# Optimization experiments

Measured on AMD Instinct MI355X. Metric: run time of the kernel, lower is better.

Reference implementation:

```python
import jax, jax.numpy as jnp
import numpy as np

OUT = 128
TYPES = [("author", 100000, 128), ("paper", 250000, 256), ("venue", 25000, 64),
         ("institution", 50000, 128), ("field", 75000, 64), ("term", 150000, 128)]


def setup_inputs() -> dict:
    key = jax.random.key(0)
    inp = {}
    for i, (name, n, f_in) in enumerate(TYPES):
        kx, kw, kb = jax.random.split(jax.random.fold_in(key, i), 3)
        inp[f"x_{name}"] = jax.random.normal(kx, (n, f_in), dtype=jnp.float32)
        # kaiming_uniform default init of torch Linear: bound = 1/sqrt(fan_in)
        bound = 1.0 / np.sqrt(f_in)
        inp[f"W_{name}"] = jax.random.uniform(kw, (OUT, f_in), dtype=jnp.float32, minval=-bound, maxval=bound)
        inp[f"b_{name}"] = jax.random.uniform(kb, (OUT,), dtype=jnp.float32, minval=-bound, maxval=bound)
    return inp


def reference(x_author, x_paper, x_venue, x_institution, x_field, x_term,
              W_author, b_author, W_paper, b_paper, W_venue, b_venue,
              W_institution, b_institution, W_field, b_field, W_term, b_term):
    # Per-type independent Linear: y_k = x_k @ W_k^T + b_k (grouped GEMM)
    def lin(x, W, b):
        return jnp.einsum('nf,of->no', x, W) + b
    return (lin(x_author, W_author, b_author),
            lin(x_paper, W_paper, b_paper),
            lin(x_venue, W_venue, b_venue),
            lin(x_institution, W_institution, b_institution),
            lin(x_field, W_field, b_field),
            lin(x_term, W_term, b_term))
```

## Files before the change

### kernel.cpp

```cpp
#include <hip/hip_runtime.h>

typedef __bf16 bf16x8 __attribute__((ext_vector_type(8)));
typedef float  f32x4  __attribute__((ext_vector_type(4)));

struct KArgs {
    const float* x[6];
    const float* W[6];
    const float* b[6];
    float*       out[6];
    int nrows[6];
    int blk0[7];
};

template<int N> __device__ __forceinline__ void wait_bar() {
    asm volatile("s_waitcnt vmcnt(%0)\n\ts_barrier" :: "n"(N) : "memory");
}
__device__ __forceinline__ void order_fence() { asm volatile("" ::: "memory"); }

__device__ __forceinline__ void gload_lds16(const float* g, void* l) {
    __builtin_amdgcn_global_load_lds(
        (const __attribute__((address_space(1))) void*)g,
        (__attribute__((address_space(3))) void*)l, 16, 0, 0);
}

template<int FIN, bool GUARD>
__device__ __forceinline__ void compute_chunk(
    const char* __restrict__ base, const bf16x8 (&Wf)[FIN/32][2],
    const f32x4 (&bv)[2], float* __restrict__ out, int nrows, int chunk,
    int l15, int lq, int colbase)
{
    constexpr int ROWS = 4096 / FIN;
    constexpr int NC   = FIN / 32;
    constexpr int MT   = ROWS / 16;
    constexpr int R    = FIN / 4;
    #pragma unroll
    for (int mt = 0; mt < MT; ++mt) {
        const int row = mt * 16 + l15;
        const int swz = row & 7;
        f32x4 acc0 = {0.f, 0.f, 0.f, 0.f};
        f32x4 acc1 = {0.f, 0.f, 0.f, 0.f};
        #pragma unroll
        for (int c = 0; c < NC; ++c) {
            const int g0 = row * R + c * 8 + lq * 2;
            const f32x4 lo = *(const f32x4*)(base + (size_t)((g0 ^ swz) << 4));
            const f32x4 hi = *(const f32x4*)(base + (size_t)(((g0 + 1) ^ swz) << 4));
            bf16x8 xf;
            xf[0]=(__bf16)lo[0]; xf[1]=(__bf16)lo[1]; xf[2]=(__bf16)lo[2]; xf[3]=(__bf16)lo[3];
            xf[4]=(__bf16)hi[0]; xf[5]=(__bf16)hi[1]; xf[6]=(__bf16)hi[2]; xf[7]=(__bf16)hi[3];
            acc0 = __builtin_amdgcn_mfma_f32_16x16x32_bf16(Wf[c][0], xf, acc0, 0, 0, 0);
            acc1 = __builtin_amdgcn_mfma_f32_16x16x32_bf16(Wf[c][1], xf, acc1, 0, 0, 0);
        }
        const int xrow = chunk * ROWS + mt * 16 + l15;
        if (!GUARD || xrow < nrows) {
            float* op = out + (size_t)xrow * 128 + colbase;
            *(f32x4*)(op + lq * 4)      = acc0 + bv[0];
            *(f32x4*)(op + 16 + lq * 4) = acc1 + bv[1];
        }
    }
}

template<int FIN>
__device__ __forceinline__ void run_type(
    const float* __restrict__ x, const float* __restrict__ W,
    const float* __restrict__ bias, float* __restrict__ out,
    int nrows, int c0, int c1, bool tail, float* __restrict__ lds)
{
    constexpr int ROWS = 4096 / FIN;
    constexpr int NC   = FIN / 32;
    constexpr int MT   = ROWS / 16;
    constexpr int R    = FIN / 4;
    constexpr int S    = 2 * MT;
    constexpr int LOGR = (FIN == 256) ? 6 : ((FIN == 128) ? 5 : 4);

    const int tid     = threadIdx.x;
    const int lane    = tid & 63;
    const int wave    = tid >> 6;
    const int l15     = lane & 15;
    const int lq      = lane >> 4;
    const int colbase = wave * 32;

    bf16x8 Wf[NC][2];
    f32x4  bv[2];
    #pragma unroll
    for (int t = 0; t < 2; ++t) {
        const int o = colbase + t * 16 + l15;
        #pragma unroll
        for (int c = 0; c < NC; ++c) {
            const f32x4 w0 = *(const f32x4*)(W + (size_t)o * FIN + c * 32 + lq * 8);
            const f32x4 w1 = *(const f32x4*)(W + (size_t)o * FIN + c * 32 + lq * 8 + 4);
            bf16x8 fr;
            fr[0]=(__bf16)w0[0]; fr[1]=(__bf16)w0[1]; fr[2]=(__bf16)w0[2]; fr[3]=(__bf16)w0[3];
            fr[4]=(__bf16)w1[0]; fr[5]=(__bf16)w1[1]; fr[6]=(__bf16)w1[2]; fr[7]=(__bf16)w1[3];
            Wf[c][t] = fr;
        }
        bv[t] = *(const f32x4*)(bias + colbase + t * 16 + lq * 4);
    }

    auto issue = [&](int chunk, int b) {
        const float* src = x + (size_t)chunk * ROWS * FIN;
        #pragma unroll
        for (int i = 0; i < 4; ++i) {
            const int G   = wave * 256 + i * 64 + lane;
            const int row = G >> LOGR;
            const int kq  = (G & (R - 1)) ^ (row & 7);
            gload_lds16(src + (size_t)row * FIN + kq * 4,
                        (char*)lds + (size_t)b * 16384 + wave * 4096 + i * 1024);
        }
    };

    const int L = c1 - c0;
    if (L > 0) {
        const int last = c1 - 1;
        order_fence();
        issue(c0, 0);
        int ch1 = c0 + 1; if (ch1 > last) ch1 = last;
        issue(ch1, 1);
        wait_bar<4>();
        int ch2 = c0 + 2; if (ch2 > last) ch2 = last;
        issue(ch2, 2);
        order_fence();
        compute_chunk<FIN, false>((const char*)lds, Wf, bv, out, nrows, c0,
                                  l15, lq, colbase);
        if (L > 1) {
            wait_bar<4 + S>();
            for (int k = 1; k < L; ++k) {
                int ch = c0 + k + 2; if (ch > last) ch = last;
                issue(ch, (k + 2) % 3);
                order_fence();
                compute_chunk<FIN, false>((const char*)lds + (size_t)(k % 3) * 16384,
                                          Wf, bv, out, nrows, c0 + k,
                                          l15, lq, colbase);
                if (k + 1 < L) wait_bar<4 + 2 * S>();
            }
        }
    }

    if (tail) {
        __syncthreads();
        const int pc = c1;
        #pragma unroll
        for (int i = 0; i < 4; ++i) {
            const int G   = wave * 256 + i * 64 + lane;
            const int row = G >> LOGR;
            const int kq  = (G & (R - 1)) ^ (row & 7);
            const int grow = pc * ROWS + row;
            if (grow < nrows) {
                const f32x4 v = *(const f32x4*)(x + (size_t)grow * FIN + kq * 4);
                *(f32x4*)((char*)lds + (size_t)G * 16) = v;
            }
        }
        __syncthreads();
        compute_chunk<FIN, true>((const char*)lds, Wf, bv, out, nrows, pc,
                                 l15, lq, colbase);
    }
}

__global__ __launch_bounds__(256, 3) void hetero_fused_kern(KArgs A)
{
    __shared__ float lds[3 * 4096];

    int ty = 0;
    const int bid = blockIdx.x;
    while (ty < 5 && bid >= A.blk0[ty + 1]) ++ty;
    const int lb = bid - A.blk0[ty];
    const int nb = A.blk0[ty + 1] - A.blk0[ty];

    const int nrows = A.nrows[ty];
    const int ROWS  = (ty == 1) ? 16 : ((ty == 2 || ty == 4) ? 64 : 32);
    const int F     = nrows / ROWS;
    const bool part = (nrows % ROWS) != 0;
    const int c0 = (int)(((long)F * lb) / nb);
    const int c1 = (int)(((long)F * (lb + 1)) / nb);
    const bool tail = part && (lb == nb - 1);

    switch (ty) {
        case 0: run_type<128>(A.x[0], A.W[0], A.b[0], A.out[0], nrows, c0, c1, tail, lds); break;
        case 1: run_type<256>(A.x[1], A.W[1], A.b[1], A.out[1], nrows, c0, c1, tail, lds); break;
        case 2: run_type< 64>(A.x[2], A.W[2], A.b[2], A.out[2], nrows, c0, c1, tail, lds); break;
        case 3: run_type<128>(A.x[3], A.W[3], A.b[3], A.out[3], nrows, c0, c1, tail, lds); break;
        case 4: run_type< 64>(A.x[4], A.W[4], A.b[4], A.out[4], nrows, c0, c1, tail, lds); break;
        case 5: run_type<128>(A.x[5], A.W[5], A.b[5], A.out[5], nrows, c0, c1, tail, lds); break;
    }
}

extern "C" void kernel_launch(void* const* d_in, const int* in_sizes, int n_in,
                              void* d_out, int out_size, void* d_ws, size_t ws_size,
                              hipStream_t stream)
{
    float* out = (float*)d_out;
    KArgs A;
    const int  nrows[6] = {100000, 250000, 25000, 50000, 75000, 150000};
    const long ooff[6]  = {0L, 12800000L, 44800000L, 48000000L, 54400000L, 64000000L};
    const int  blk0[7]  = {0, 273, 1297, 1348, 1485, 1639, 2048};
    for (int t = 0; t < 6; ++t) {
        A.x[t]     = (const float*)d_in[3 * t + 0];
        A.W[t]     = (const float*)d_in[3 * t + 1];
        A.b[t]     = (const float*)d_in[3 * t + 2];
        A.out[t]   = out + ooff[t];
        A.nrows[t] = nrows[t];
    }
    for (int i = 0; i < 7; ++i) A.blk0[i] = blk0[i];

    hetero_fused_kern<<<2048, 256, 0, stream>>>(A);
}
```

Measured before the change: 165.3 us.

## Split each block into producer and consumer waves for warp-specialised pipelining

Blocks grow to 512 threads. Four producer waves only stream x chunks into the triple-buffered LDS ring with global_load_lds, and four consumer waves hold the bf16 weight fragments and run the MFMA compute and stores. The aim is to stop each wave alternating between issuing loads and computing, so loads and math overlap more cleanly. The grid is halved to 1024 blocks and the per-type block offsets are rescaled to match. The cost is more LDS barriers per chunk, fewer compute waves per CU, and register or LDS limits that may hold occupancy below the launch-bounds target.

```diff
diff --git a/kernel.cpp b/kernel.cpp
--- a/kernel.cpp
+++ b/kernel.cpp
@@ -12,10 +12,12 @@
     int blk0[7];
 };
 
-template<int N> __device__ __forceinline__ void wait_bar() {
-    asm volatile("s_waitcnt vmcnt(%0)\n\ts_barrier" :: "n"(N) : "memory");
-}
-__device__ __forceinline__ void order_fence() { asm volatile("" ::: "memory"); }
+__device__ __forceinline__ void prod_wait_bar() {
+    asm volatile("s_waitcnt vmcnt(4)\n\ts_barrier" ::: "memory");
+}
+__device__ __forceinline__ void cons_bar() {
+    asm volatile("s_waitcnt lgkmcnt(0)\n\ts_barrier" ::: "memory");
+}
 
 __device__ __forceinline__ void gload_lds16(const float* g, void* l) {
     __builtin_amdgcn_global_load_lds(
@@ -67,71 +69,71 @@
 {
     constexpr int ROWS = 4096 / FIN;
     constexpr int NC   = FIN / 32;
-    constexpr int MT   = ROWS / 16;
     constexpr int R    = FIN / 4;
-    constexpr int S    = 2 * MT;
     constexpr int LOGR = (FIN == 256) ? 6 : ((FIN == 128) ? 5 : 4);
 
-    const int tid     = threadIdx.x;
-    const int lane    = tid & 63;
-    const int wave    = tid >> 6;
-    const int l15     = lane & 15;
-    const int lq      = lane >> 4;
-    const int colbase = wave * 32;
-
-    bf16x8 Wf[NC][2];
-    f32x4  bv[2];
-    #pragma unroll
-    for (int t = 0; t < 2; ++t) {
-        const int o = colbase + t * 16 + l15;
+    const int tid  = threadIdx.x;
+    const int lane = tid & 63;
+    const int wave = tid >> 6;
+    const int l15  = lane & 15;
+    const int lq   = lane >> 4;
+    const bool is_prod = (wave < 4);
+
+    const int L    = c1 - c0;
+    const int last = c1 - 1;
+
+    if (is_prod) {
+        const int pw = wave;
+        auto issue = [&](int chunk, int slot) {
+            const float* src = x + (size_t)chunk * ROWS * FIN;
+            #pragma unroll
+            for (int i = 0; i < 4; ++i) {
+                const int G   = pw * 256 + i * 64 + lane;
+                const int row = G >> LOGR;
+                const int kq  = (G & (R - 1)) ^ (row & 7);
+                gload_lds16(src + (size_t)row * FIN + kq * 4,
+                            (char*)lds + (size_t)slot * 16384 + pw * 4096 + i * 1024);
+            }
+        };
+        if (L > 0) {
+            issue(c0, c0 % 3);
+            int ch1 = c0 + 1; if (ch1 > last) ch1 = last;
+            issue(ch1, (c0 + 1) % 3);
+            prod_wait_bar();
+            for (int k = c0; k < c1; ++k) {
+                int ch = k + 2; if (ch > last) ch = last;
+                issue(ch, (k + 2) % 3);
+                prod_wait_bar();
+            }
+        }
+    } else {
+        const int colbase = (wave - 4) * 32;
+        bf16x8 Wf[NC][2];
+        f32x4  bv[2];
         #pragma unroll
-        for (int c = 0; c < NC; ++c) {
-            const f32x4 w0 = *(const f32x4*)(W + (size_t)o * FIN + c * 32 + lq * 8);
-            const f32x4 w1 = *(const f32x4*)(W + (size_t)o * FIN + c * 32 + lq * 8 + 4);
-            bf16x8 fr;
-            fr[0]=(__bf16)w0[0]; fr[1]=(__bf16)w0[1]; fr[2]=(__bf16)w0[2]; fr[3]=(__bf16)w0[3];
-            fr[4]=(__bf16)w1[0]; fr[5]=(__bf16)w1[1]; fr[6]=(__bf16)w1[2]; fr[7]=(__bf16)w1[3];
-            Wf[c][t] = fr;
-        }
-        bv[t] = *(const f32x4*)(bias + colbase + t * 16 + lq * 4);
-    }
-
-    auto issue = [&](int chunk, int b) {
-        const float* src = x + (size_t)chunk * ROWS * FIN;
-        #pragma unroll
-        for (int i = 0; i < 4; ++i) {
-            const int G   = wave * 256 + i * 64 + lane;
-            const int row = G >> LOGR;
-            const int kq  = (G & (R - 1)) ^ (row & 7);
-            gload_lds16(src + (size_t)row * FIN + kq * 4,
-                        (char*)lds + (size_t)b * 16384 + wave * 4096 + i * 1024);
-        }
-    };
-
-    const int L = c1 - c0;
-    if (L > 0) {
-        const int last = c1 - 1;
-        order_fence();
-        issue(c0, 0);
-        int ch1 = c0 + 1; if (ch1 > last) ch1 = last;
-        issue(ch1, 1);
-        wait_bar<4>();
-        int ch2 = c0 + 2; if (ch2 > last) ch2 = last;
-        issue(ch2, 2);
-        order_fence();
-        compute_chunk<FIN, false>((const char*)lds, Wf, bv, out, nrows, c0,
-                                  l15, lq, colbase);
-        if (L > 1) {
-            wait_bar<4 + S>();
-            for (int k = 1; k < L; ++k) {
-                int ch = c0 + k + 2; if (ch > last) ch = last;
-                issue(ch, (k + 2) % 3);
-                order_fence();
-                compute_chunk<FIN, false>((const char*)lds + (size_t)(k % 3) * 16384,
-                                          Wf, bv, out, nrows, c0 + k,
-                                          l15, lq, colbase);
-                if (k + 1 < L) wait_bar<4 + 2 * S>();
-            }
+        for (int t = 0; t < 2; ++t) {
+            const int o = colbase + t * 16 + l15;
+            #pragma unroll
+            for (int c = 0; c < NC; ++c) {
+                const f32x4 w0 = *(const f32x4*)(W + (size_t)o * FIN + c * 32 + lq * 8);
+                const f32x4 w1 = *(const f32x4*)(W + (size_t)o * FIN + c * 32 + lq * 8 + 4);
+                bf16x8 fr;
+                fr[0]=(__bf16)w0[0]; fr[1]=(__bf16)w0[1]; fr[2]=(__bf16)w0[2]; fr[3]=(__bf16)w0[3];
+                fr[4]=(__bf16)w1[0]; fr[5]=(__bf16)w1[1]; fr[6]=(__bf16)w1[2]; fr[7]=(__bf16)w1[3];
+                Wf[c][t] = fr;
+            }
+            bv[t] = *(const f32x4*)(bias + colbase + t * 16 + lq * 4);
+        }
+        if (L > 0) {
+            cons_bar();
+            for (int k = c0; k < c1; ++k) {
+                compute_chunk<FIN, false>(
+                    (const char*)lds + (size_t)(k % 3) * 16384,
+                    Wf, bv, out, nrows, k, l15, lq, colbase);
+                cons_bar();
+            }
+        }
+        if (tail) {
         }
     }
 
@@ -139,8 +141,8 @@
         __syncthreads();
         const int pc = c1;
         #pragma unroll
-        for (int i = 0; i < 4; ++i) {
-            const int G   = wave * 256 + i * 64 + lane;
+        for (int i = 0; i < 2; ++i) {
+            const int G   = tid + i * 512;
             const int row = G >> LOGR;
             const int kq  = (G & (R - 1)) ^ (row & 7);
             const int grow = pc * ROWS + row;
@@ -150,12 +152,31 @@
             }
         }
         __syncthreads();
-        compute_chunk<FIN, true>((const char*)lds, Wf, bv, out, nrows, pc,
-                                 l15, lq, colbase);
-    }
-}
-
-__global__ __launch_bounds__(256, 3) void hetero_fused_kern(KArgs A)
+        if (!is_prod) {
+            const int colbase = (wave - 4) * 32;
+            bf16x8 Wf[NC][2];
+            f32x4  bv[2];
+            #pragma unroll
+            for (int t = 0; t < 2; ++t) {
+                const int o = colbase + t * 16 + l15;
+                #pragma unroll
+                for (int c = 0; c < NC; ++c) {
+                    const f32x4 w0 = *(const f32x4*)(W + (size_t)o * FIN + c * 32 + lq * 8);
+                    const f32x4 w1 = *(const f32x4*)(W + (size_t)o * FIN + c * 32 + lq * 8 + 4);
+                    bf16x8 fr;
+                    fr[0]=(__bf16)w0[0]; fr[1]=(__bf16)w0[1]; fr[2]=(__bf16)w0[2]; fr[3]=(__bf16)w0[3];
+                    fr[4]=(__bf16)w1[0]; fr[5]=(__bf16)w1[1]; fr[6]=(__bf16)w1[2]; fr[7]=(__bf16)w1[3];
+                    Wf[c][t] = fr;
+                }
+                bv[t] = *(const f32x4*)(bias + colbase + t * 16 + lq * 4);
+            }
+            compute_chunk<FIN, true>((const char*)lds, Wf, bv, out, nrows, pc,
+                                     l15, lq, colbase);
+        }
+    }
+}
+
+__global__ __launch_bounds__(512, 4) void hetero_fused_kern(KArgs A)
 {
     __shared__ float lds[3 * 4096];
 
@@ -191,7 +212,7 @@
     KArgs A;
     const int  nrows[6] = {100000, 250000, 25000, 50000, 75000, 150000};
     const long ooff[6]  = {0L, 12800000L, 44800000L, 48000000L, 54400000L, 64000000L};
-    const int  blk0[7]  = {0, 273, 1297, 1348, 1485, 1639, 2048};
+    const int  blk0[7]  = {0, 137, 649, 674, 742, 819, 1024};
     for (int t = 0; t < 6; ++t) {
         A.x[t]     = (const float*)d_in[3 * t + 0];
         A.W[t]     = (const float*)d_in[3 * t + 1];
@@ -201,5 +222,5 @@
     }
     for (int i = 0; i < 7; ++i) A.blk0[i] = blk0[i];
 
-    hetero_fused_kern<<<2048, 256, 0, stream>>>(A);
-}
+    hetero_fused_kern<<<1024, 512, 0, stream>>>(A);
+}
```

Measured after the change: 159.1 us. -3.7%, faster.
